# Performance work log

Measured on AMD Instinct MI355X. Metric: run time of the kernel, lower is better.

Reference implementation:

```python
import jax, jax.numpy as jnp
import numpy as np

N = 10000       # nodes
E = 160000      # edges
B = 100         # graphs
F_NODE = 32
F_EDGE = 16
H0, H1, H2, H3, H4, H5 = 32, 64, 128, 256, 128, 64
EPS = 1e-5


def setup_inputs() -> dict:
    key = jax.random.key(0)
    ks = jax.random.split(key, 32)

    def rn(k, shape):
        fan_in = shape[0] if len(shape) > 1 else shape[0]
        return jax.random.normal(k, shape, jnp.float32) / np.float32(np.sqrt(fan_in))

    inp = {}
    inp["x"] = jax.random.normal(ks[0], (N, F_NODE), jnp.float32)
    inp["edge_index"] = jax.random.randint(ks[1], (2, E), 0, N)
    inp["edge_attr"] = jax.random.normal(ks[2], (E, F_EDGE), jnp.float32)
    inp["batch"] = jnp.sort(jax.random.randint(ks[3], (N,), 0, B))
    # EdgeMLP: F_EDGE -> 128 -> 64 -> F_NODE*H0
    inp["We1"] = rn(ks[4], (F_EDGE, 128)); inp["be1"] = jnp.zeros((128,), jnp.float32)
    inp["We2"] = rn(ks[5], (128, 64));     inp["be2"] = jnp.zeros((64,), jnp.float32)
    inp["We3"] = rn(ks[6], (64, F_NODE * H0)); inp["be3"] = jnp.zeros((F_NODE * H0,), jnp.float32)
    # NNConv root linear + bias
    inp["Wroot"] = rn(ks[7], (F_NODE, H0)); inp["bc1"] = jnp.zeros((H0,), jnp.float32)
    # GATConv 1 (H0 -> H1, heads=1)
    inp["Wg1"] = rn(ks[8], (H0, H1)); inp["as1"] = rn(ks[9], (H1,)); inp["ad1"] = rn(ks[10], (H1,)); inp["bg1"] = jnp.zeros((H1,), jnp.float32)
    # GATConv 2 (H1 -> H2, heads=1)
    inp["Wg2"] = rn(ks[11], (H1, H2)); inp["as2"] = rn(ks[12], (H2,)); inp["ad2"] = rn(ks[13], (H2,)); inp["bg2"] = jnp.zeros((H2,), jnp.float32)
    # FC head
    inp["Wf1"] = rn(ks[14], (H2, H3)); inp["bf1"] = jnp.zeros((H3,), jnp.float32)
    inp["Wf2"] = rn(ks[15], (H3, H4)); inp["bf2"] = jnp.zeros((H4,), jnp.float32)
    inp["Wf3"] = rn(ks[16], (H4, H5)); inp["bf3"] = jnp.zeros((H5,), jnp.float32)
    return inp


def _bn(h):  # training-mode BatchNorm1d, affine = identity (default init)
    m = h.mean(axis=0)
    v = h.var(axis=0)
    return (h - m) * jax.lax.rsqrt(v + EPS)


def _seg_softmax(e, seg, n):
    m = jax.ops.segment_max(e, seg, num_segments=n)
    ex = jnp.exp(e - m[seg])
    s = jax.ops.segment_sum(ex, seg, num_segments=n)
    return ex / (s[seg] + 1e-16)


def _gat(x, src, dst, W, a_src, a_dst, b):
    n = x.shape[0]
    h = x @ W                                     # [N, F_out]
    loop = jnp.arange(n)                          # PyG add_self_loops=True
    s = jnp.concatenate([src, loop])
    d = jnp.concatenate([dst, loop])
    sc_s = h @ a_src                              # [N]
    sc_d = h @ a_dst
    e = jax.nn.leaky_relu(sc_s[s] + sc_d[d], negative_slope=0.2)
    alpha = _seg_softmax(e, d, n)                 # segment softmax over in-edges
    out = jax.ops.segment_sum(alpha[:, None] * h[s], d, num_segments=n)
    return out + b


def reference(x, edge_index, edge_attr, batch,
              We1, be1, We2, be2, We3, be3, Wroot, bc1,
              Wg1, as1, ad1, bg1, Wg2, as2, ad2, bg2,
              Wf1, bf1, Wf2, bf2, Wf3, bf3):
    src, dst = edge_index[0], edge_index[1]

    # --- NNConv: per-edge weight matrices from EdgeMLP ---
    t = jax.nn.relu(edge_attr @ We1 + be1)
    t = jax.nn.relu(t @ We2 + be2)
    theta = (t @ We3 + be3).reshape(E, F_NODE, H0)        # [E, F_in, F_out]
    msg = jnp.einsum('ef,efo->eo', x[src], theta)          # gather-matmul
    agg = jax.ops.segment_sum(msg, dst, num_segments=N)    # scatter-add (aggr='add')
    h = agg + x @ Wroot + bc1
    h = jax.nn.relu(_bn(h))

    # --- GATConv x2 ---
    h = jax.nn.relu(_bn(_gat(h, src, dst, Wg1, as1, ad1, bg1)))
    h = jax.nn.relu(_bn(_gat(h, src, dst, Wg2, as2, ad2, bg2)))

    # --- global mean pool ---
    sums = jax.ops.segment_sum(h, batch, num_segments=B)
    cnts = jax.ops.segment_sum(jnp.ones((N,), h.dtype), batch, num_segments=B)
    g = sums / jnp.maximum(cnts, 1.0)[:, None]             # [B, H2]

    # --- MLP head (dropout=Identity in eval/reference) ---
    g = jax.nn.relu(_bn(g @ Wf1 + bf1))
    g = jax.nn.relu(_bn(g @ Wf2 + bf2))
    return g @ Wf3 + bf3                                   # [B, H5]
```

## Files before the change

kernel.cpp:

```cpp
#include <hip/hip_runtime.h>

#define NN 10000
#define NE 160000
#define NGB 100

typedef __attribute__((ext_vector_type(8))) short s8v;
typedef __attribute__((ext_vector_type(4))) float f4v;
typedef __attribute__((ext_vector_type(2))) _Float16 h2v;

static __device__ __forceinline__ float lrelu(float v){ return v > 0.f ? v : 0.2f*v; }
static __device__ __forceinline__ unsigned short f2bf(float f){
  unsigned u = __float_as_uint(f);
  u += 0x7fffu + ((u >> 16) & 1u);
  return (unsigned short)(u >> 16);
}
static __device__ __forceinline__ float bf2f(unsigned short h){
  return __uint_as_float(((unsigned)h) << 16);
}
static __device__ __forceinline__ unsigned pkh(float a, float b){
  auto h = __builtin_amdgcn_cvt_pkrtz(a, b);
  return __builtin_bit_cast(unsigned, h);
}
static __device__ __forceinline__ unsigned short f2h(float f){
  _Float16 h = (_Float16)f;
  return __builtin_bit_cast(unsigned short, h);
}
static __device__ __forceinline__ float h2f(unsigned short u){
  return (float)__builtin_bit_cast(_Float16, u);
}
static __device__ __forceinline__ float dot2h(unsigned t, unsigned y, float acc){
#if __has_builtin(__builtin_amdgcn_fdot2)
  return __builtin_amdgcn_fdot2(__builtin_bit_cast(h2v, t), __builtin_bit_cast(h2v, y), acc, false);
#else
  h2v a = __builtin_bit_cast(h2v, t), b = __builtin_bit_cast(h2v, y);
  return acc + (float)a[0]*(float)b[0] + (float)a[1]*(float)b[1];
#endif
}

__global__ __launch_bounds__(256) void k_deg_bounds(const int* __restrict__ src, const int* __restrict__ dst,
                                                    const int* __restrict__ batch,
                                                    int* deg_src, int* deg_dst, int* starts){
  int i = blockIdx.x*256 + threadIdx.x;
  if (i < NE){ atomicAdd(&deg_src[src[i]],1); atomicAdd(&deg_dst[dst[i]],1); }
  if (i <= NN){
    int cur  = (i==NN) ? NGB : batch[i];
    int prev = (i==0)  ? -1  : batch[i-1];
    for (int b=prev+1; b<=cur; b++) if (b<=NGB) starts[b]=i;
  }
}

__global__ __launch_bounds__(1024) void k_scan(const int* __restrict__ deg_src, const int* __restrict__ deg_dst,
                                               int* rp_src, int* rp_dst){
  const int* deg = (blockIdx.x==0) ? deg_src : deg_dst;
  int* rp = (blockIdx.x==0) ? rp_src : rp_dst;
  __shared__ int part[1024];
  int tid = threadIdx.x;
  const int per = (NN + 1023)/1024;
  int base = tid*per;
  int s = 0;
  for (int i=0;i<per;i++){ int idx=base+i; if (idx<NN) s += deg[idx]; }
  part[tid]=s; __syncthreads();
  for (int off=1; off<1024; off<<=1){
    int v = part[tid];
    int add = (tid>=off) ? part[tid-off] : 0;
    __syncthreads();
    part[tid] = v + add;
    __syncthreads();
  }
  int run = (tid==0) ? 0 : part[tid-1];
  for (int i=0;i<per;i++){ int idx=base+i; if (idx<NN){ rp[idx]=run; run += deg[idx]; } }
  if (tid==1023) rp[NN] = part[1023];
}

__global__ __launch_bounds__(256) void k_fill(const int* __restrict__ src, const int* __restrict__ dst,
                       const int* __restrict__ rp_src, const int* __restrict__ rp_dst,
                       int* fill_src, int* fill_dst, int* pos_src, int* dstp, int* srcd, int* dstd){
  int i = blockIdx.x*256 + threadIdx.x;
  if (i < NE){
    int s=src[i], d=dst[i];
    int p=rp_src[s]+atomicAdd(&fill_src[s],1); pos_src[i]=p; dstp[p]=d;
    int q=rp_dst[d]+atomicAdd(&fill_dst[d],1); srcd[q]=s; dstd[q]=d;
  }
}

__global__ __launch_bounds__(256) void k_packall(const float* __restrict__ We1, const float* __restrict__ be1,
    const float* __restrict__ We2, const float* __restrict__ We3,
    unsigned short* __restrict__ W1p, unsigned short* __restrict__ W2p,
    unsigned short* __restrict__ W3h, unsigned short* __restrict__ W3l){
  int tid = threadIdx.x;
  if (blockIdx.x == 32){
    for (int idx=tid; idx<512; idx+=256){
      int j=idx>>6, l=idx&63, col=l&15, g=l>>4;
      int out = j*16+col;
      #pragma unroll
      for (int jj=0;jj<8;jj++){
        int k = g*8+jj;
        float v = (k<16) ? We1[k*128+out] : (k==16 ? be1[out] : 0.f);
        W1p[idx*8+jj] = f2bf(v);
      }
    }
    for (int idx=tid; idx<1024; idx+=256){
      int ft=idx>>6, l=idx&63, col=l&15, g=l>>4;
      int t=ft>>2, jo=ft&3;
      int out = jo*16+col;
      #pragma unroll
      for (int jj=0;jj<8;jj++){
        int k = t*32+g*8+jj;
        W2p[idx*8+jj] = f2bf(We2[k*64+out]);
      }
    }
  } else {
    int idx = blockIdx.x*256 + tid;
    int jt = idx>>6, l = idx&63;
    int j = jt*16 + (l&15);
    int f0 = (l>>4)*8;
    int k = j>>5, o = j&31;
    #pragma unroll
    for (int jj=0;jj<8;jj++){
      float v = We3[(size_t)k*1024 + (size_t)(f0+jj)*32 + o];
      unsigned short h = f2bf(v);
      float r = v - bf2f(h);
      W3h[(size_t)idx*8+jj] = h;
      W3l[(size_t)idx*8+jj] = f2bf(r);
    }
  }
}

__global__ __launch_bounds__(256) void k_edge_mlp2(const float* __restrict__ ea,
    const unsigned short* __restrict__ W1p, const unsigned short* __restrict__ W2p,
    const float* __restrict__ be2, const int* __restrict__ pos_src, unsigned* __restrict__ t2b){
  __shared__ unsigned short st1[4*2048];
  int tid=threadIdx.x, wave=tid>>6, lane=tid&63;
  int c = lane&15, g = lane>>4;
  s8v w1f[8], w2f[16];
  #pragma unroll
  for (int j=0;j<8;j++)  w1f[j] = *(const s8v*)(W1p + (size_t)(j*64+lane)*8);
  #pragma unroll
  for (int q=0;q<16;q++) w2f[q] = *(const s8v*)(W2p + (size_t)(q*64+lane)*8);
  float be2v[16];
  #pragma unroll
  for (int jo=0;jo<4;jo++)
    #pragma unroll
    for (int r=0;r<4;r++) be2v[jo*4+r] = be2[jo*16+g*4+r];
  char* myld = (char*)(st1 + wave*2048);
  const f4v fzero = {0.f,0.f,0.f,0.f};

  for (int base = blockIdx.x*64; base < NE; base += gridDim.x*64){
    int e0 = base + wave*16;
    s8v eaf = {0,0,0,0,0,0,0,0};
    if (g < 2){
      const float* p = ea + (size_t)(e0+c)*16 + g*8;
      float4 a = *(const float4*)p;
      float4 b = *(const float4*)(p+4);
      eaf[0]=(short)f2bf(a.x); eaf[1]=(short)f2bf(a.y); eaf[2]=(short)f2bf(a.z); eaf[3]=(short)f2bf(a.w);
      eaf[4]=(short)f2bf(b.x); eaf[5]=(short)f2bf(b.y); eaf[6]=(short)f2bf(b.z); eaf[7]=(short)f2bf(b.w);
    } else if (g == 2){
      eaf[0] = (short)0x3f80;
    }
    f4v acc1[8];
    #pragma unroll
    for (int j=0;j<8;j++)
      acc1[j] = __builtin_amdgcn_mfma_f32_16x16x32_bf16(w1f[j], eaf, fzero, 0, 0, 0);
    #pragma unroll
    for (int j=0;j<8;j++){
      unsigned lo = (unsigned)f2bf(fmaxf(acc1[j][0],0.f)) | ((unsigned)f2bf(fmaxf(acc1[j][1],0.f))<<16);
      unsigned hi = (unsigned)f2bf(fmaxf(acc1[j][2],0.f)) | ((unsigned)f2bf(fmaxf(acc1[j][3],0.f))<<16);
      unsigned off = (unsigned)(c*256 + ((j*32 + g*8) ^ (c<<4)));
      *(uint2*)(myld + off) = make_uint2(lo, hi);
    }
    __syncthreads();
    f4v acc2[4];
    #pragma unroll
    for (int jo=0;jo<4;jo++) acc2[jo] = fzero;
    #pragma unroll
    for (int t=0;t<4;t++){
      unsigned off = (unsigned)(c*256 + ((t*64 + g*16) ^ (c<<4)));
      s8v b2 = *(const s8v*)(myld + off);
      #pragma unroll
      for (int jo=0;jo<4;jo++)
        acc2[jo] = __builtin_amdgcn_mfma_f32_16x16x32_bf16(w2f[t*4+jo], b2, acc2[jo], 0, 0, 0);
    }
    int pos = pos_src[e0+c];
    unsigned* orow = t2b + (size_t)pos*32;
    #pragma unroll
    for (int jo=0;jo<4;jo++){
      float v0 = fmaxf(acc2[jo][0] + be2v[jo*4+0], 0.f);
      float v1 = fmaxf(acc2[jo][1] + be2v[jo*4+1], 0.f);
      float v2 = fmaxf(acc2[jo][2] + be2v[jo*4+2], 0.f);
      float v3 = fmaxf(acc2[jo][3] + be2v[jo*4+3], 0.f);
      *(uint2*)(orow + jo*8 + g*2) = make_uint2(pkh(v0,v1), pkh(v2,v3));
    }
    __syncthreads();
  }
}

__global__ __launch_bounds__(256) void k_y6(const float* __restrict__ x,
    const unsigned short* __restrict__ W3h, const unsigned short* __restrict__ W3l,
    unsigned* __restrict__ Yp){
  int tid=threadIdx.x, w=tid>>6, l=tid&63;
  int c = l&15, g = l>>4;
  int tile = blockIdx.x*2 + (w>>1);
  if (tile >= 625) return;
  int jhalf = w&1;
  int n = tile*16 + c;
  const float* xr = x + (size_t)n*32 + g*8;
  float4 xa = *(const float4*)xr;
  float4 xc = *(const float4*)(xr+4);
  float xv[8] = {xa.x,xa.y,xa.z,xa.w,xc.x,xc.y,xc.z,xc.w};
  s8v bh, bl;
  #pragma unroll
  for (int jj=0;jj<8;jj++){
    unsigned short h = f2bf(xv[jj]);
    bh[jj] = (short)h;
    bl[jj] = (short)f2bf(xv[jj] - bf2f(h));
  }
  const f4v fz = {0.f,0.f,0.f,0.f};
  unsigned* Yrow = Yp + (size_t)n*1024;
  for (int grp=0; grp<4; grp++){
    int jt_g0 = jhalf*64 + grp*16;
    int kpg = jhalf*4 + grp;
    uint4 Q[2][4];
    #pragma unroll
    for (int a=0; a<4; a++){
      #pragma unroll
      for (int b=0; b<2; b++){
        int jt_lo = jt_g0 + 4*a + b;
        int jt_hi = jt_lo + 2;
        s8v AhL = *(const s8v*)(W3h + (size_t)(jt_lo*64 + l)*8);
        s8v AlL = *(const s8v*)(W3l + (size_t)(jt_lo*64 + l)*8);
        f4v aL = __builtin_amdgcn_mfma_f32_16x16x32_bf16(AhL, bl, fz, 0, 0, 0);
        aL = __builtin_amdgcn_mfma_f32_16x16x32_bf16(AlL, bh, aL, 0, 0, 0);
        aL = __builtin_amdgcn_mfma_f32_16x16x32_bf16(AhL, bh, aL, 0, 0, 0);
        s8v AhH = *(const s8v*)(W3h + (size_t)(jt_hi*64 + l)*8);
        s8v AlH = *(const s8v*)(W3l + (size_t)(jt_hi*64 + l)*8);
        f4v aH = __builtin_amdgcn_mfma_f32_16x16x32_bf16(AhH, bl, fz, 0, 0, 0);
        aH = __builtin_amdgcn_mfma_f32_16x16x32_bf16(AlH, bh, aH, 0, 0, 0);
        aH = __builtin_amdgcn_mfma_f32_16x16x32_bf16(AhH, bh, aH, 0, 0, 0);
        #pragma unroll
        for (int r=0;r<4;r++){
          unsigned pv = pkh(aL[r], aH[r]);
          if (a==0) Q[b][r].x = pv;
          else if (a==1) Q[b][r].y = pv;
          else if (a==2) Q[b][r].z = pv;
          else Q[b][r].w = pv;
        }
      }
    }
    #pragma unroll
    for (int b=0;b<2;b++)
      #pragma unroll
      for (int r=0;r<4;r++){
        int o = b*16 + g*4 + r;
        *(uint4*)(Yrow + kpg*128 + o*4) = Q[b][r];
      }
  }
}

__global__ __launch_bounds__(256) void k_xbagg(const float* __restrict__ x,
    const float* __restrict__ be3, const float* __restrict__ Wroot, const float* __restrict__ bc1,
    float* __restrict__ xb, float* __restrict__ agg){
  __shared__ __align__(16) float sx[8][32];
  int oo = threadIdx.x & 31, nn = threadIdx.x >> 5;
  float wb[32], wr[32];
  #pragma unroll
  for (int f=0;f<32;f++){ wb[f]=be3[f*32+oo]; wr[f]=Wroot[f*32+oo]; }
  float bcv = bc1[oo];
  int per = (1250 + gridDim.x - 1)/gridDim.x;
  int g0 = blockIdx.x*per, g1 = min(g0+per, 1250);
  for (int gi=g0; gi<g1; gi++){
    int nb = gi*8;
    __syncthreads();
    sx[threadIdx.x>>5][threadIdx.x&31] = x[(size_t)nb*32 + threadIdx.x];
    __syncthreads();
    float a1=0.f, a2=0.f;
    #pragma unroll
    for (int f4=0;f4<8;f4++){
      float4 xvv = *(const float4*)(&sx[nn][f4*4]);
      a1 += xvv.x*wb[f4*4+0]+xvv.y*wb[f4*4+1]+xvv.z*wb[f4*4+2]+xvv.w*wb[f4*4+3];
      a2 += xvv.x*wr[f4*4+0]+xvv.y*wr[f4*4+1]+xvv.z*wr[f4*4+2]+xvv.w*wr[f4*4+3];
    }
    xb[(size_t)(nb+nn)*32+oo] = a1;
    agg[(size_t)(nb+nn)*32+oo] = a2 + bcv;
  }
}

__global__ __launch_bounds__(256) void k_msg3(const unsigned* __restrict__ Yp,
    const float* __restrict__ xb, const unsigned* __restrict__ t2b,
    const int* __restrict__ rp_src, const int* __restrict__ dstp,
    float* __restrict__ agg){
  __shared__ __align__(16) unsigned sY[4][1024];
  int tid=threadIdx.x, w=tid>>6, lane=tid&63;
  int es = lane>>4, l = lane&15;
  int gw = blockIdx.x*4 + w, stride = gridDim.x*4;
  for (int n=gw; n<NN; n+=stride){
    int beg=rp_src[n], end=rp_src[n+1];
    if (beg==end) continue;
    const unsigned* Yr = Yp + (size_t)n*1024;
    #pragma unroll
    for (int q=0;q<4;q++){
      uint4 v = *(const uint4*)(Yr + q*256 + lane*4);
      int U = q*64 + lane;
      int kpg_ = U>>5, o_ = U&31;
      int T = o_*8 + ((kpg_ + (o_>>1)) & 7);
      *(uint4*)(&sY[w][T*4]) = v;
    }
    float2 xbv = *(const float2*)(xb + (size_t)n*32 + 2*l);
    __builtin_amdgcn_wave_barrier();
    for (int pb=beg; pb<end; pb+=4){
      const unsigned* trow = t2b + (size_t)(pb+es)*32;
      uint4 T[8];
      #pragma unroll
      for (int q=0;q<8;q++) T[q] = *(const uint4*)(trow + q*4);
      float acc0 = xbv.x, acc1 = xbv.y;
      #pragma unroll
      for (int kpg=0;kpg<8;kpg++){
        int slot4 = ((kpg + l)&7)*4;
        uint4 y0 = *(const uint4*)(&sY[w][(2*l  )*32 + slot4]);
        uint4 y1 = *(const uint4*)(&sY[w][(2*l+1)*32 + slot4]);
        acc0 = dot2h(T[kpg].x, y0.x, acc0);
        acc0 = dot2h(T[kpg].y, y0.y, acc0);
        acc0 = dot2h(T[kpg].z, y0.z, acc0);
        acc0 = dot2h(T[kpg].w, y0.w, acc0);
        acc1 = dot2h(T[kpg].x, y1.x, acc1);
        acc1 = dot2h(T[kpg].y, y1.y, acc1);
        acc1 = dot2h(T[kpg].z, y1.z, acc1);
        acc1 = dot2h(T[kpg].w, y1.w, acc1);
      }
      int p = pb + es;
      if (p < end){
        int d = dstp[p];
        float* ap = agg + (size_t)d*32 + 2*l;
        unsafeAtomicAdd(ap,   acc0);
        unsafeAtomicAdd(ap+1, acc1);
      }
    }
  }
}

__global__ __launch_bounds__(256) void k_stats(const float* __restrict__ buf, int nrows, int ncols,
                                               float* __restrict__ stats){
  int tid = threadIdx.x;
  int c  = tid % ncols;
  int r0 = tid / ncols;
  int rp = 256 / ncols;
  float s1=0.f, s2=0.f;
  for (long long base=(long long)blockIdx.x*rp; base<nrows; base+=(long long)gridDim.x*rp){
    int r = (int)base + r0;
    if (r < nrows){
      float v = buf[(size_t)r*ncols + c];
      s1 += v; s2 += v*v;
    }
  }
  __shared__ float A[256], B[256];
  A[tid]=s1; B[tid]=s2; __syncthreads();
  if (tid < ncols){
    float t1=0.f, t2=0.f;
    for (int gg=0; gg<256/ncols; gg++){ t1 += A[gg*ncols+tid]; t2 += B[gg*ncols+tid]; }
    atomicAdd(&stats[tid], t1);
    atomicAdd(&stats[ncols+tid], t2);
  }
}

template<int FIN, int FOUT>
__global__ __launch_bounds__(256) void k_gat_linear(const float* __restrict__ raw,
    const float* __restrict__ stats, const float* __restrict__ W,
    const float* __restrict__ avs, const float* __restrict__ avd,
    unsigned short* __restrict__ hWh, float* __restrict__ sc_s, float* __restrict__ sc_d){
  __shared__ float sW[FIN*FOUT];
  __shared__ float sA[FOUT], sD[FOUT];
  __shared__ float sScale[FIN], sShift[FIN];
  __shared__ float sIn[4][FIN];
  int tid = threadIdx.x;
  for (int i=tid;i<FIN*FOUT;i+=256) sW[i]=W[i];
  if (tid<FOUT){ sA[tid]=avs[tid]; sD[tid]=avd[tid]; }
  if (tid<FIN){
    float m = stats[tid]*(1.f/NN);
    float v = stats[FIN+tid]*(1.f/NN) - m*m;
    float s = rsqrtf(v + 1e-5f);
    sScale[tid]=s; sShift[tid]=-m*s;
  }
  __syncthreads();
  int wave=tid>>6, lane=tid&63;
  for (int nb = blockIdx.x*4; nb < NN; nb += gridDim.x*4){
    int n = nb + wave;
    bool act = n < NN;
    if (act){
      for (int ff=lane; ff<FIN; ff+=64){
        float vv = raw[(size_t)n*FIN+ff]*sScale[ff]+sShift[ff];
        sIn[wave][ff] = fmaxf(vv, 0.f);
      }
    }
    __syncthreads();
    if (act){
      float out0=0.f, out1=0.f;
      #pragma unroll
      for (int ff=0; ff<FIN; ff++){
        float xv = sIn[wave][ff];
        out0 += xv*sW[ff*FOUT+lane];
        if constexpr (FOUT > 64) out1 += xv*sW[ff*FOUT+lane+64];
      }
      hWh[(size_t)n*FOUT + lane] = f2h(out0);
      float ps = out0*sA[lane], pd = out0*sD[lane];
      if constexpr (FOUT > 64){
        hWh[(size_t)n*FOUT + lane + 64] = f2h(out1);
        ps += out1*sA[lane+64]; pd += out1*sD[lane+64];
      }
      #pragma unroll
      for (int off=32;off>0;off>>=1){ ps += __shfl_down(ps,off); pd += __shfl_down(pd,off); }
      if (lane==0){ sc_s[n]=ps; sc_d[n]=pd; }
    }
    __syncthreads();
  }
}

__global__ __launch_bounds__(256) void k_escore(const float* __restrict__ sc_s, const float* __restrict__ sc_d,
    const int* __restrict__ srcd, const int* __restrict__ dstd, float* __restrict__ sce){
  int q = blockIdx.x*256 + threadIdx.x;
  if (q < NE) sce[q] = lrelu(sc_s[srcd[q]] + sc_d[dstd[q]]);
}

template<int F>
__global__ __launch_bounds__(256) void k_gat_attn4(const unsigned short* __restrict__ hWh,
    const float* __restrict__ sce, const float* __restrict__ sc_s, const float* __restrict__ sc_d,
    const int* __restrict__ rp_dst, const int* __restrict__ srcd,
    const float* __restrict__ bias, float* __restrict__ outraw){
  int tid=threadIdx.x, w=tid>>6, lane=tid&63;
  int gw = blockIdx.x*4 + w, stride = gridDim.x*4;
  for (int n=gw; n<NN; n+=stride){
    int beg=rp_dst[n], end=rp_dst[n+1];
    float M=-3e38f, S=0.f, acc0=0.f, acc1=0.f;
    for (int base=beg; base<end; base+=64){
      int nb = min(64, end-base);
      float sc=-3e38f; int si=0;
      if (lane<nb){ sc = sce[base+lane]; si = srcd[base+lane]; }
      float cm=sc;
      #pragma unroll
      for (int off=32;off>0;off>>=1) cm = fmaxf(cm, __shfl_xor(cm,off));
      float Mn = fmaxf(M, cm);
      float p = (lane<nb) ? __expf(sc-Mn) : 0.f;
      float ps=p;
      #pragma unroll
      for (int off=32;off>0;off>>=1) ps += __shfl_xor(ps,off);
      float scale = __expf(M-Mn);
      S = S*scale + ps;
      acc0*=scale; acc1*=scale;
      int jj=0;
      for (; jj+4<=nb; jj+=4){
        float p0=__shfl(p,jj), p1=__shfl(p,jj+1), p2=__shfl(p,jj+2), p3=__shfl(p,jj+3);
        int   q0=__shfl(si,jj), q1=__shfl(si,jj+1), q2=__shfl(si,jj+2), q3=__shfl(si,jj+3);
        if constexpr (F==128){
          unsigned u0 = *(const unsigned*)(hWh + (size_t)q0*128 + 2*lane);
          unsigned u1 = *(const unsigned*)(hWh + (size_t)q1*128 + 2*lane);
          unsigned u2 = *(const unsigned*)(hWh + (size_t)q2*128 + 2*lane);
          unsigned u3 = *(const unsigned*)(hWh + (size_t)q3*128 + 2*lane);
          acc0 += p0*h2f((unsigned short)(u0&0xffffu)); acc1 += p0*h2f((unsigned short)(u0>>16));
          acc0 += p1*h2f((unsigned short)(u1&0xffffu)); acc1 += p1*h2f((unsigned short)(u1>>16));
          acc0 += p2*h2f((unsigned short)(u2&0xffffu)); acc1 += p2*h2f((unsigned short)(u2>>16));
          acc0 += p3*h2f((unsigned short)(u3&0xffffu)); acc1 += p3*h2f((unsigned short)(u3>>16));
        } else {
          float v0 = h2f(hWh[(size_t)q0*64+lane]);
          float v1 = h2f(hWh[(size_t)q1*64+lane]);
          float v2 = h2f(hWh[(size_t)q2*64+lane]);
          float v3 = h2f(hWh[(size_t)q3*64+lane]);
          acc0 += p0*v0 + p1*v1 + p2*v2 + p3*v3;
        }
      }
      for (; jj<nb; jj++){
        float pj=__shfl(p,jj); int qj=__shfl(si,jj);
        if constexpr (F==128){
          unsigned u = *(const unsigned*)(hWh + (size_t)qj*128 + 2*lane);
          acc0 += pj*h2f((unsigned short)(u&0xffffu));
          acc1 += pj*h2f((unsigned short)(u>>16));
        } else {
          acc0 += pj*h2f(hWh[(size_t)qj*64+lane]);
        }
      }
      M = Mn;
    }
    float sself = lrelu(sc_s[n]+sc_d[n]);
    float Mn = fmaxf(M, sself);
    float scale = __expf(M-Mn);
    float pself = __expf(sself-Mn);
    S = S*scale + pself;
    acc0*=scale; acc1*=scale;
    float inv = 1.f/(S+1e-16f);
    if constexpr (F==128){
      unsigned u = *(const unsigned*)(hWh + (size_t)n*128 + 2*lane);
      acc0 += pself*h2f((unsigned short)(u&0xffffu));
      acc1 += pself*h2f((unsigned short)(u>>16));
      float ox = acc0*inv + bias[2*lane];
      float oy = acc1*inv + bias[2*lane+1];
      *(float2*)(outraw + (size_t)n*128 + 2*lane) = make_float2(ox, oy);
    } else {
      acc0 += pself*h2f(hWh[(size_t)n*64+lane]);
      outraw[(size_t)n*64+lane] = acc0*inv + bias[lane];
    }
  }
}

__global__ __launch_bounds__(256) void k_pool(const float* __restrict__ h2raw,
    const float* __restrict__ stats, const int* __restrict__ starts,
    float* __restrict__ g){
  __shared__ float sc[128], sh[128];
  __shared__ float red[256];
  int b=blockIdx.x, t=threadIdx.x;
  if (t<128){
    float m = stats[t]*(1.f/NN);
    float v = stats[128+t]*(1.f/NN) - m*m;
    float s = rsqrtf(v+1e-5f);
    sc[t]=s; sh[t]=-m*s;
  }
  __syncthreads();
  int s0=starts[b], s1=starts[b+1];
  int f=t&127, half=t>>7;
  float acc=0.f;
  for (int n=s0+half;n<s1;n+=2){
    float v = h2raw[(size_t)n*128+f]*sc[f]+sh[f];
    acc += fmaxf(v,0.f);
  }
  red[t]=acc; __syncthreads();
  if (half==0){
    int cnt = s1-s0;
    g[b*128+f] = (red[f]+red[128+f]) / fmaxf((float)cnt, 1.f);
  }
}

__global__ __launch_bounds__(256) void k_head1(const float* __restrict__ g,
    const float* __restrict__ Wf1, const float* __restrict__ bf1, float* __restrict__ g1,
    float* __restrict__ statsH1){
  __shared__ float sg[128];
  int r=blockIdx.x, t=threadIdx.x;
  if (t<128) sg[t]=g[r*128+t];
  __syncthreads();
  float acc=bf1[t];
  #pragma unroll 4
  for (int k=0;k<128;k++) acc += sg[k]*Wf1[k*256+t];
  g1[r*256+t]=acc;
  atomicAdd(&statsH1[t], acc);
  atomicAdd(&statsH1[256+t], acc*acc);
}

__global__ __launch_bounds__(256) void k_head2(const float* __restrict__ g1,
    const float* __restrict__ stats, const float* __restrict__ Wf2,
    const float* __restrict__ bf2, float* __restrict__ g2, float* __restrict__ statsH2){
  __shared__ float sin_[256];
  int r=blockIdx.x, t=threadIdx.x;
  float m = stats[t]*(1.f/NGB);
  float v = stats[256+t]*(1.f/NGB) - m*m;
  float val = (g1[r*256+t]-m)*rsqrtf(v+1e-5f);
  sin_[t]=fmaxf(val,0.f);
  __syncthreads();
  if (t<128){
    float acc=bf2[t];
    #pragma unroll 4
    for (int k=0;k<256;k++) acc += sin_[k]*Wf2[k*128+t];
    g2[r*128+t]=acc;
    atomicAdd(&statsH2[t], acc);
    atomicAdd(&statsH2[128+t], acc*acc);
  }
}

__global__ __launch_bounds__(256) void k_head3(const float* __restrict__ g2,
    const float* __restrict__ stats, const float* __restrict__ Wf3,
    const float* __restrict__ bf3, float* __restrict__ out){
  __shared__ float sin_[128];
  int r=blockIdx.x, t=threadIdx.x;
  if (t<128){
    float m = stats[t]*(1.f/NGB);
    float v = stats[128+t]*(1.f/NGB) - m*m;
    float val = (g2[r*128+t]-m)*rsqrtf(v+1e-5f);
    sin_[t]=fmaxf(val,0.f);
  }
  __syncthreads();
  if (t<64){
    float acc=bf3[t];
    #pragma unroll 4
    for (int k=0;k<128;k++) acc += sin_[k]*Wf3[k*64+t];
    out[r*64+t]=acc;
  }
}

extern "C" void kernel_launch(void* const* d_in, const int* in_sizes, int n_in,
                              void* d_out, int out_size, void* d_ws, size_t ws_size,
                              hipStream_t stream){
  const float* x    = (const float*)d_in[0];
  const int*   ei   = (const int*)d_in[1];
  const float* ea   = (const float*)d_in[2];
  const int*   batch= (const int*)d_in[3];
  const float* We1=(const float*)d_in[4];  const float* be1=(const float*)d_in[5];
  const float* We2=(const float*)d_in[6];  const float* be2=(const float*)d_in[7];
  const float* We3=(const float*)d_in[8];  const float* be3=(const float*)d_in[9];
  const float* Wroot=(const float*)d_in[10]; const float* bc1=(const float*)d_in[11];
  const float* Wg1=(const float*)d_in[12]; const float* as1=(const float*)d_in[13];
  const float* ad1=(const float*)d_in[14]; const float* bg1=(const float*)d_in[15];
  const float* Wg2=(const float*)d_in[16]; const float* as2=(const float*)d_in[17];
  const float* ad2=(const float*)d_in[18]; const float* bg2=(const float*)d_in[19];
  const float* Wf1=(const float*)d_in[20]; const float* bf1=(const float*)d_in[21];
  const float* Wf2=(const float*)d_in[22]; const float* bf2=(const float*)d_in[23];
  const float* Wf3=(const float*)d_in[24]; const float* bf3=(const float*)d_in[25];
  (void)in_sizes; (void)n_in; (void)out_size; (void)ws_size;
  float* out = (float*)d_out;
  char* ws = (char*)d_ws;
  const int* srcA = ei;
  const int* dstA = ei + NE;

  size_t off = 0;
  auto take = [&](size_t bytes)->size_t{ size_t r = off; off += (bytes + 255) & ~(size_t)255; return r; };
  size_t o_deg_src = take(NN*4), o_deg_dst = take(NN*4);
  size_t o_fill_src = take(NN*4), o_fill_dst = take(NN*4);
  size_t o_stats0 = take(2*32*4), o_stats1 = take(2*64*4), o_stats2 = take(2*128*4);
  size_t o_statsH1 = take(2*256*4), o_statsH2 = take(2*128*4);
  size_t zero_bytes = off;
  size_t o_rp_src = take((NN+1)*4), o_rp_dst = take((NN+1)*4);
  size_t o_pos_src = take((size_t)NE*4);
  size_t o_dstp = take((size_t)NE*4);
  size_t o_srcd = take((size_t)NE*4);
  size_t o_dstd = take((size_t)NE*4);
  size_t o_sce  = take((size_t)NE*4);
  size_t o_starts = take((NGB+1)*4);
  size_t o_W1p = take(4096*2);
  size_t o_W2p = take(8192*2);
  size_t o_W3h = take((size_t)128*64*8*2);
  size_t o_W3l = take((size_t)128*64*8*2);
  size_t o_t2b = take((size_t)(NE+8)*32*4);
  size_t o_Yp  = take((size_t)NN*1024*4);
  size_t o_xb  = take((size_t)NN*32*4);
  size_t o_agg = take((size_t)NN*32*4);
  size_t o_hW1 = take((size_t)NN*64*2);
  size_t o_scs1 = take(NN*4), o_scd1 = take(NN*4);
  size_t o_h1  = take((size_t)NN*64*4);
  size_t o_hW2 = take((size_t)NN*128*2);
  size_t o_scs2 = take(NN*4), o_scd2 = take(NN*4);
  size_t o_h2  = take((size_t)NN*128*4);
  size_t o_g   = take(NGB*128*4);
  size_t o_g1  = take(NGB*256*4);
  size_t o_g2  = take(NGB*128*4);

  #define WF(o) ((float*)(ws + (o)))
  #define WI(o) ((int*)(ws + (o)))
  #define WU(o) ((unsigned short*)(ws + (o)))
  #define WW(o) ((unsigned*)(ws + (o)))

  (void)hipMemsetAsync(ws, 0, zero_bytes, stream);
  k_deg_bounds<<<625,256,0,stream>>>(srcA,dstA,batch,WI(o_deg_src),WI(o_deg_dst),WI(o_starts));
  k_scan<<<2,1024,0,stream>>>(WI(o_deg_src),WI(o_deg_dst),WI(o_rp_src),WI(o_rp_dst));
  k_fill<<<625,256,0,stream>>>(srcA,dstA,WI(o_rp_src),WI(o_rp_dst),
                               WI(o_fill_src),WI(o_fill_dst),
                               WI(o_pos_src),WI(o_dstp),WI(o_srcd),WI(o_dstd));
  k_packall<<<33,256,0,stream>>>(We1,be1,We2,We3,WU(o_W1p),WU(o_W2p),WU(o_W3h),WU(o_W3l));
  k_edge_mlp2<<<500,256,0,stream>>>(ea,WU(o_W1p),WU(o_W2p),be2,WI(o_pos_src),WW(o_t2b));
  k_y6<<<313,256,0,stream>>>(x,WU(o_W3h),WU(o_W3l),WW(o_Yp));
  k_xbagg<<<256,256,0,stream>>>(x,be3,Wroot,bc1,WF(o_xb),WF(o_agg));
  k_msg3<<<2500,256,0,stream>>>(WW(o_Yp),WF(o_xb),WW(o_t2b),WI(o_rp_src),WI(o_dstp),WF(o_agg));

  k_stats<<<64,256,0,stream>>>(WF(o_agg),NN,32,WF(o_stats0));
  k_gat_linear<32,64><<<640,256,0,stream>>>(WF(o_agg),WF(o_stats0),Wg1,as1,ad1,
                                            WU(o_hW1),WF(o_scs1),WF(o_scd1));
  k_escore<<<625,256,0,stream>>>(WF(o_scs1),WF(o_scd1),WI(o_srcd),WI(o_dstd),WF(o_sce));
  k_gat_attn4<64><<<2500,256,0,stream>>>(WU(o_hW1),WF(o_sce),WF(o_scs1),WF(o_scd1),
                                         WI(o_rp_dst),WI(o_srcd),bg1,WF(o_h1));
  k_stats<<<64,256,0,stream>>>(WF(o_h1),NN,64,WF(o_stats1));
  k_gat_linear<64,128><<<640,256,0,stream>>>(WF(o_h1),WF(o_stats1),Wg2,as2,ad2,
                                             WU(o_hW2),WF(o_scs2),WF(o_scd2));
  k_escore<<<625,256,0,stream>>>(WF(o_scs2),WF(o_scd2),WI(o_srcd),WI(o_dstd),WF(o_sce));
  k_gat_attn4<128><<<2500,256,0,stream>>>(WU(o_hW2),WF(o_sce),WF(o_scs2),WF(o_scd2),
                                          WI(o_rp_dst),WI(o_srcd),bg2,WF(o_h2));
  k_stats<<<64,256,0,stream>>>(WF(o_h2),NN,128,WF(o_stats2));

  k_pool<<<NGB,256,0,stream>>>(WF(o_h2),WF(o_stats2),WI(o_starts),WF(o_g));
  k_head1<<<NGB,256,0,stream>>>(WF(o_g),Wf1,bf1,WF(o_g1),WF(o_statsH1));
  k_head2<<<NGB,256,0,stream>>>(WF(o_g1),WF(o_statsH1),Wf2,bf2,WF(o_g2),WF(o_statsH2));
  k_head3<<<NGB,256,0,stream>>>(WF(o_g2),WF(o_statsH2),Wf3,bf3,out);
}
```

Measured before the change: 304.6 us.

## Compute per-edge NNConv messages with MFMA f16 instead of dot2 loops

Replaces the per-source-node message kernel's LDS-staged fdot2 inner loop with 16x16x32 f16 MFMA instructions. Each wave now handles 16 edges per iteration and keeps the node's Y block in registers as B fragments, which removes the shared-memory staging. The t2b edge buffer padding grows to 16 rows to cover the wider edge tiles. The cost is that nodes with few outgoing edges (about 16 on average) waste part of each 16-row tile, and the atomic scatter pattern changes to per-column lanes.

```diff
diff --git a/kernel.cpp b/kernel.cpp
--- a/kernel.cpp
+++ b/kernel.cpp
@@ -7,6 +7,7 @@
 typedef __attribute__((ext_vector_type(8))) short s8v;
 typedef __attribute__((ext_vector_type(4))) float f4v;
 typedef __attribute__((ext_vector_type(2))) _Float16 h2v;
+typedef __attribute__((ext_vector_type(8))) _Float16 h8v;
 
 static __device__ __forceinline__ float lrelu(float v){ return v > 0.f ? v : 0.2f*v; }
 static __device__ __forceinline__ unsigned short f2bf(float f){
@@ -27,14 +28,6 @@
 }
 static __device__ __forceinline__ float h2f(unsigned short u){
   return (float)__builtin_bit_cast(_Float16, u);
-}
-static __device__ __forceinline__ float dot2h(unsigned t, unsigned y, float acc){
-#if __has_builtin(__builtin_amdgcn_fdot2)
-  return __builtin_amdgcn_fdot2(__builtin_bit_cast(h2v, t), __builtin_bit_cast(h2v, y), acc, false);
-#else
-  h2v a = __builtin_bit_cast(h2v, t), b = __builtin_bit_cast(h2v, y);
-  return acc + (float)a[0]*(float)b[0] + (float)a[1]*(float)b[1];
-#endif
 }
 
 __global__ __launch_bounds__(256) void k_deg_bounds(const int* __restrict__ src, const int* __restrict__ dst,
@@ -284,54 +277,43 @@
   }
 }
 
-__global__ __launch_bounds__(256) void k_msg3(const unsigned* __restrict__ Yp,
+__global__ __launch_bounds__(256) void k_msg4(const unsigned* __restrict__ Yp,
     const float* __restrict__ xb, const unsigned* __restrict__ t2b,
     const int* __restrict__ rp_src, const int* __restrict__ dstp,
     float* __restrict__ agg){
-  __shared__ __align__(16) unsigned sY[4][1024];
   int tid=threadIdx.x, w=tid>>6, lane=tid&63;
-  int es = lane>>4, l = lane&15;
+  int c = lane&15, g = lane>>4;
   int gw = blockIdx.x*4 + w, stride = gridDim.x*4;
+  const f4v fz = {0.f,0.f,0.f,0.f};
   for (int n=gw; n<NN; n+=stride){
     int beg=rp_src[n], end=rp_src[n+1];
     if (beg==end) continue;
     const unsigned* Yr = Yp + (size_t)n*1024;
-    #pragma unroll
-    for (int q=0;q<4;q++){
-      uint4 v = *(const uint4*)(Yr + q*256 + lane*4);
-      int U = q*64 + lane;
-      int kpg_ = U>>5, o_ = U&31;
-      int T = o_*8 + ((kpg_ + (o_>>1)) & 7);
-      *(uint4*)(&sY[w][T*4]) = v;
-    }
-    float2 xbv = *(const float2*)(xb + (size_t)n*32 + 2*l);
-    __builtin_amdgcn_wave_barrier();
-    for (int pb=beg; pb<end; pb+=4){
-      const unsigned* trow = t2b + (size_t)(pb+es)*32;
-      uint4 T[8];
-      #pragma unroll
-      for (int q=0;q<8;q++) T[q] = *(const uint4*)(trow + q*4);
-      float acc0 = xbv.x, acc1 = xbv.y;
-      #pragma unroll
-      for (int kpg=0;kpg<8;kpg++){
-        int slot4 = ((kpg + l)&7)*4;
-        uint4 y0 = *(const uint4*)(&sY[w][(2*l  )*32 + slot4]);
-        uint4 y1 = *(const uint4*)(&sY[w][(2*l+1)*32 + slot4]);
-        acc0 = dot2h(T[kpg].x, y0.x, acc0);
-        acc0 = dot2h(T[kpg].y, y0.y, acc0);
-        acc0 = dot2h(T[kpg].z, y0.z, acc0);
-        acc0 = dot2h(T[kpg].w, y0.w, acc0);
-        acc1 = dot2h(T[kpg].x, y1.x, acc1);
-        acc1 = dot2h(T[kpg].y, y1.y, acc1);
-        acc1 = dot2h(T[kpg].z, y1.z, acc1);
-        acc1 = dot2h(T[kpg].w, y1.w, acc1);
-      }
-      int p = pb + es;
-      if (p < end){
-        int d = dstp[p];
-        float* ap = agg + (size_t)d*32 + 2*l;
-        unsafeAtomicAdd(ap,   acc0);
-        unsafeAtomicAdd(ap+1, acc1);
+    h8v B[2][2];
+    #pragma unroll
+    for (int kt=0;kt<2;kt++)
+      #pragma unroll
+      for (int jn=0;jn<2;jn++)
+        B[kt][jn] = __builtin_bit_cast(h8v, *(const uint4*)(Yr + (kt*4+g)*128 + (jn*16+c)*4));
+    float xq0 = xb[(size_t)n*32 + c];
+    float xq1 = xb[(size_t)n*32 + c + 16];
+    for (int eb=beg; eb<end; eb+=16){
+      const unsigned* tr = t2b + (size_t)(eb + c)*32;
+      h8v A0 = __builtin_bit_cast(h8v, *(const uint4*)(tr + g*4));
+      h8v A1 = __builtin_bit_cast(h8v, *(const uint4*)(tr + 16 + g*4));
+      f4v acc0 = __builtin_amdgcn_mfma_f32_16x16x32_f16(A0, B[0][0], fz, 0, 0, 0);
+      acc0 = __builtin_amdgcn_mfma_f32_16x16x32_f16(A1, B[1][0], acc0, 0, 0, 0);
+      f4v acc1 = __builtin_amdgcn_mfma_f32_16x16x32_f16(A0, B[0][1], fz, 0, 0, 0);
+      acc1 = __builtin_amdgcn_mfma_f32_16x16x32_f16(A1, B[1][1], acc1, 0, 0, 0);
+      #pragma unroll
+      for (int r=0;r<4;r++){
+        int p = eb + g*4 + r;
+        if (p < end){
+          int d = dstp[p];
+          float* ap = agg + (size_t)d*32;
+          unsafeAtomicAdd(ap + c,      acc0[r] + xq0);
+          unsafeAtomicAdd(ap + c + 16, acc1[r] + xq1);
+        }
       }
     }
   }
@@ -622,7 +604,7 @@
   size_t o_W2p = take(8192*2);
   size_t o_W3h = take((size_t)128*64*8*2);
   size_t o_W3l = take((size_t)128*64*8*2);
-  size_t o_t2b = take((size_t)(NE+8)*32*4);
+  size_t o_t2b = take((size_t)(NE+16)*32*4);
   size_t o_Yp  = take((size_t)NN*1024*4);
   size_t o_xb  = take((size_t)NN*32*4);
   size_t o_agg = take((size_t)NN*32*4);
@@ -651,7 +633,7 @@
   k_edge_mlp2<<<500,256,0,stream>>>(ea,WU(o_W1p),WU(o_W2p),be2,WI(o_pos_src),WW(o_t2b));
   k_y6<<<313,256,0,stream>>>(x,WU(o_W3h),WU(o_W3l),WW(o_Yp));
   k_xbagg<<<256,256,0,stream>>>(x,be3,Wroot,bc1,WF(o_xb),WF(o_agg));
-  k_msg3<<<2500,256,0,stream>>>(WW(o_Yp),WF(o_xb),WW(o_t2b),WI(o_rp_src),WI(o_dstp),WF(o_agg));
+  k_msg4<<<2500,256,0,stream>>>(WW(o_Yp),WF(o_xb),WW(o_t2b),WI(o_rp_src),WI(o_dstp),WF(o_agg));
 
   k_stats<<<64,256,0,stream>>>(WF(o_agg),NN,32,WF(o_stats0));
   k_gat_linear<32,64><<<640,256,0,stream>>>(WF(o_agg),WF(o_stats0),Wg1,as1,ad1,
```

Result: faster. 288.4 us (-5.3%).
